# Performance work log

Measured on AMD Instinct MI355X. Metric: run time of the kernel, lower is better.

Reference implementation:

```python
import jax, jax.numpy as jnp
import numpy as np

N_NODES = 100000
N_EDGES = 3200000
N_IN = 128
N_HID = 128
N_OUT = 64
HOP = 10


def setup_inputs() -> dict:
    key = jax.random.key(0)
    ks = jax.random.split(key, 8)
    x = jax.random.normal(ks[0], (N_NODES, N_IN), dtype=jnp.float32)
    edge_row = jax.random.randint(ks[1], (N_EDGES,), 0, N_NODES, dtype=jnp.int32)
    edge_col = jax.random.randint(ks[2], (N_EDGES,), 0, N_NODES, dtype=jnp.int32)
    # normalized-ish edge weights so 10 hops of propagation stay bounded
    edge_val = jax.random.uniform(ks[3], (N_EDGES,), dtype=jnp.float32) / 32.0
    s_ih = 1.0 / np.sqrt(N_IN)
    s_hh = 1.0 / np.sqrt(N_HID)
    W_ih = jax.random.normal(ks[4], (4 * N_HID, N_IN), dtype=jnp.float32) * s_ih
    W_hh = jax.random.normal(ks[5], (4 * N_HID, N_HID), dtype=jnp.float32) * s_hh
    b_ih = jnp.zeros((4 * N_HID,), dtype=jnp.float32)
    b_hh = jnp.zeros((4 * N_HID,), dtype=jnp.float32)
    fc_w = jax.random.normal(ks[6], (N_OUT, N_HID), dtype=jnp.float32) * s_hh
    fc_b = jnp.zeros((N_OUT,), dtype=jnp.float32)
    return dict(x=x, edge_row=edge_row, edge_col=edge_col, edge_val=edge_val,
                W_ih=W_ih, W_hh=W_hh, b_ih=b_ih, b_hh=b_hh, fc_w=fc_w, fc_b=fc_b)


def _lstm_cell(x, h, c, W_ih, W_hh, b_ih, b_hh):
    # torch LSTMCell gate order: input, forget, cell(g), output
    gates = x @ W_ih.T + b_ih + h @ W_hh.T + b_hh  # [N, 4H]
    i, f, g, o = jnp.split(gates, 4, axis=-1)
    i = jax.nn.sigmoid(i)
    f = jax.nn.sigmoid(f)
    g = jnp.tanh(g)
    o = jax.nn.sigmoid(o)
    c_new = f * c + i * g
    h_new = o * jnp.tanh(c_new)
    return h_new, c_new


def _spmm(edge_row, edge_col, edge_val, h, n_nodes):
    # (A @ h)[r] = sum_{edges e with row r} val[e] * h[col[e]]
    msgs = edge_val[:, None] * h[edge_col]  # [E, H] gather
    return jax.ops.segment_sum(msgs, edge_row, num_segments=n_nodes)


def reference(x, edge_row, edge_col, edge_val, W_ih, W_hh, b_ih, b_hh, fc_w, fc_b):
    n = x.shape[0]
    h = jnp.zeros((n, W_hh.shape[1]), dtype=x.dtype)
    c = jnp.zeros_like(h)
    # hop iterations: LSTM gate update then sparse propagation (dropout = eval/identity)
    for _ in range(HOP):
        h, c = _lstm_cell(x, h, c, W_ih, W_hh, b_ih, b_hh)
        h = _spmm(edge_row, edge_col, edge_val, h, n)
    h = jax.nn.relu(h)
    return h @ fc_w.T + fc_b
```

## Files before the change

### kernel.cpp

```cpp
#include <hip/hip_runtime.h>
#include <hip/hip_bf16.h>
#include <math.h>

constexpr int NN  = 100000;
constexpr int EE  = 3200000;
constexpr int HID = 128;
constexpr int NG  = 512;
constexpr int NOUT = 64;
constexpr int HOPS = 10;

typedef __attribute__((ext_vector_type(8))) short short8;
typedef __attribute__((ext_vector_type(4))) float f32x4;

__device__ __forceinline__ ushort f2bf(float f) {
    uint u = __builtin_bit_cast(uint, f);
    u += 0x7fff + ((u >> 16) & 1);
    return (ushort)(u >> 16);
}
__device__ __forceinline__ float bflo(uint u) { return __builtin_bit_cast(float, u << 16); }
__device__ __forceinline__ float bfhi(uint u) { return __builtin_bit_cast(float, u & 0xffff0000u); }

__device__ __forceinline__ float sigf(float v) { return 1.0f / (1.0f + __expf(-v)); }
__device__ __forceinline__ float tanh_fast(float x) {
    float t = __expf(-2.0f * fabsf(x));
    float r = (1.0f - t) / (1.0f + t);
    return copysignf(r, x);
}

__device__ __forceinline__ short8 load_frag(const ushort* p) {
    return *reinterpret_cast<const short8*>(p);
}
__device__ __forceinline__ f32x4 mfma16(short8 a, short8 b, f32x4 c) {
    return __builtin_amdgcn_mfma_f32_16x16x32_bf16(a, b, c, 0, 0, 0);
}

__global__ __launch_bounds__(256) void convert_bf16_kernel(
    const float* __restrict__ src, ushort* __restrict__ dst, int n4)
{
    int i = blockIdx.x * 256 + threadIdx.x;
    if (i < n4) {
        float4 v = reinterpret_cast<const float4*>(src)[i];
        ushort4 o;
        o.x = f2bf(v.x); o.y = f2bf(v.y); o.z = f2bf(v.z); o.w = f2bf(v.w);
        reinterpret_cast<ushort4*>(dst)[i] = o;
    }
}

__global__ __launch_bounds__(256) void bsum_kernel(
    const float* __restrict__ bih, const float* __restrict__ bhh, float* __restrict__ bsum)
{
    int i = blockIdx.x * 256 + threadIdx.x;
    if (i < NG) bsum[i] = bih[i] + bhh[i];
}

__global__ __launch_bounds__(256) void hist_kernel(const int* __restrict__ erow,
                                                   int* __restrict__ deg)
{
    int e = blockIdx.x * 256 + threadIdx.x;
    atomicAdd(&deg[erow[e]], 1);
}

__global__ __launch_bounds__(1024) void scan_kernel(const int* __restrict__ deg,
                                                    int* __restrict__ rp,
                                                    int* __restrict__ cur)
{
    __shared__ int tmp[1024];
    __shared__ int carry_s;
    int t = threadIdx.x;
    if (t == 0) { carry_s = 0; rp[0] = 0; }
    __syncthreads();
    for (int base = 0; base < NN; base += 1024) {
        int i = base + t;
        int v = (i < NN) ? deg[i] : 0;
        tmp[t] = v;
        __syncthreads();
        for (int off = 1; off < 1024; off <<= 1) {
            int add = (t >= off) ? tmp[t - off] : 0;
            __syncthreads();
            tmp[t] += add;
            __syncthreads();
        }
        int incl = tmp[t] + carry_s;
        if (i < NN) { rp[i + 1] = incl; cur[i] = incl - v; }
        __syncthreads();
        if (t == 1023) carry_s = incl;
        __syncthreads();
    }
}

__global__ __launch_bounds__(256) void scatter_kernel(
    const int* __restrict__ erow, const int* __restrict__ ecol,
    const float* __restrict__ eval, int* __restrict__ cur,
    int* __restrict__ scol, float* __restrict__ sval)
{
    int e = blockIdx.x * 256 + threadIdx.x;
    int r = erow[e];
    int p = atomicAdd(&cur[r], 1);
    scol[p] = ecol[e];
    sval[p] = eval[e];
}

template<bool FIRST>
__global__ __launch_bounds__(256, 2) void cell_kernel(
    const ushort* __restrict__ xb, const ushort* __restrict__ hb,
    const ushort* __restrict__ Wib, const ushort* __restrict__ Whb,
    const float* __restrict__ bsum, float* __restrict__ cperm,
    ushort* __restrict__ hout)
{
    __shared__ __align__(16) ushort lds_h[32 * 136];

    const int t  = threadIdx.x;
    const int l  = t & 63;
    const int w  = t >> 6;
    const int lr = l & 15;
    const int lk = l >> 4;
    const int row0 = blockIdx.x * 32;

    f32x4 acc[8][2];
#pragma unroll
    for (int nI = 0; nI < 8; ++nI) {
        float b = bsum[(4 * nI + w) * 16 + lr];
        acc[nI][0] = f32x4{b, b, b, b};
        acc[nI][1] = f32x4{b, b, b, b};
    }

    short8 ax[2][4];
    short8 ah[2][4];
#pragma unroll
    for (int rf = 0; rf < 2; ++rf) {
        const size_t arow = (size_t)(row0 + rf * 16 + lr) * HID + lk * 8;
#pragma unroll
        for (int ks = 0; ks < 4; ++ks) {
            ax[rf][ks] = load_frag(xb + arow + ks * 32);
            if (!FIRST) ah[rf][ks] = load_frag(hb + arow + ks * 32);
        }
    }

#pragma unroll
    for (int nI = 0; nI < 8; ++nI) {
        const int n = 4 * nI + w;
        const ushort* wip = Wib + (size_t)(n * 16 + lr) * HID + lk * 8;
        const ushort* whp = Whb + (size_t)(n * 16 + lr) * HID + lk * 8;
        short8 bi[4], bh[4];
#pragma unroll
        for (int ks = 0; ks < 4; ++ks) {
            bi[ks] = load_frag(wip + ks * 32);
            if (!FIRST) bh[ks] = load_frag(whp + ks * 32);
        }
#pragma unroll
        for (int rf = 0; rf < 2; ++rf) {
#pragma unroll
            for (int ks = 0; ks < 4; ++ks) {
                acc[nI][rf] = mfma16(ax[rf][ks], bi[ks], acc[nI][rf]);
                if (!FIRST) acc[nI][rf] = mfma16(ah[rf][ks], bh[ks], acc[nI][rf]);
            }
        }
    }

#pragma unroll
    for (int nj = 0; nj < 2; ++nj) {
        const int col = (w + 4 * nj) * 16 + lr;
#pragma unroll
        for (int rf = 0; rf < 2; ++rf) {
            f32x4 iv = acc[nj][rf];
            f32x4 fv = acc[nj + 2][rf];
            f32x4 gv = acc[nj + 4][rf];
            f32x4 ov = acc[nj + 6][rf];
            const size_t cidx = ((((size_t)blockIdx.x * 4 + w) * 2 + nj) * 2 + rf) * 64 + l;
            f32x4 cold;
            if (FIRST) cold = f32x4{0.f, 0.f, 0.f, 0.f};
            else       cold = reinterpret_cast<const f32x4*>(cperm)[cidx];
            f32x4 cn, hn;
#pragma unroll
            for (int jj = 0; jj < 4; ++jj) {
                float c2 = sigf(fv[jj]) * cold[jj] + sigf(iv[jj]) * tanh_fast(gv[jj]);
                cn[jj] = c2;
                hn[jj] = sigf(ov[jj]) * tanh_fast(c2);
            }
            reinterpret_cast<f32x4*>(cperm)[cidx] = cn;
            const int rbase = rf * 16 + lk * 4;
#pragma unroll
            for (int jj = 0; jj < 4; ++jj)
                lds_h[(rbase + jj) * 136 + col] = f2bf(hn[jj]);
        }
    }
    __syncthreads();
    {
        const ushort* lsrc = &lds_h[(t >> 3) * 136 + (t & 7) * 16];
        short8 v0 = *reinterpret_cast<const short8*>(lsrc);
        short8 v1 = *reinterpret_cast<const short8*>(lsrc + 8);
        ushort* gdst = hout + (size_t)row0 * HID + t * 16;
        *reinterpret_cast<short8*>(gdst) = v0;
        *reinterpret_cast<short8*>(gdst + 8) = v1;
    }
}

__global__ __launch_bounds__(256) void spmm_kernel(
    const int* __restrict__ rp, const int* __restrict__ scol,
    const float* __restrict__ sval, const ushort* __restrict__ hin,
    ushort* __restrict__ hout)
{
    int r = blockIdx.x * 4 + (threadIdx.x >> 6);
    if (r >= NN) return;
    int l = threadIdx.x & 63;
    int beg = rp[r], end = rp[r + 1];

    float s0a = 0.f, s1a = 0.f, s0b = 0.f, s1b = 0.f;
    float s0c = 0.f, s1c = 0.f, s0d = 0.f, s1d = 0.f;
    int e = beg;
    for (; e + 4 <= end; e += 4) {
        int c0 = scol[e], c1 = scol[e + 1], c2 = scol[e + 2], c3 = scol[e + 3];
        float v0 = sval[e], v1 = sval[e + 1], v2 = sval[e + 2], v3 = sval[e + 3];
        uint g0 = *reinterpret_cast<const uint*>(hin + (size_t)c0 * HID + l * 2);
        uint g1 = *reinterpret_cast<const uint*>(hin + (size_t)c1 * HID + l * 2);
        uint g2 = *reinterpret_cast<const uint*>(hin + (size_t)c2 * HID + l * 2);
        uint g3 = *reinterpret_cast<const uint*>(hin + (size_t)c3 * HID + l * 2);
        s0a += v0 * bflo(g0); s1a += v0 * bfhi(g0);
        s0b += v1 * bflo(g1); s1b += v1 * bfhi(g1);
        s0c += v2 * bflo(g2); s1c += v2 * bfhi(g2);
        s0d += v3 * bflo(g3); s1d += v3 * bfhi(g3);
    }
    for (; e < end; ++e) {
        int c0 = scol[e];
        float v0 = sval[e];
        uint g0 = *reinterpret_cast<const uint*>(hin + (size_t)c0 * HID + l * 2);
        s0a += v0 * bflo(g0); s1a += v0 * bfhi(g0);
    }
    float s0 = (s0a + s0b) + (s0c + s0d);
    float s1 = (s1a + s1b) + (s1c + s1d);
    uint o = ((uint)f2bf(s1) << 16) | (uint)f2bf(s0);
    *reinterpret_cast<uint*>(hout + (size_t)r * HID + l * 2) = o;
}

__global__ __launch_bounds__(256) void final_mfma_kernel(
    const ushort* __restrict__ hb, const ushort* __restrict__ fcwb,
    const float* __restrict__ fcb, float* __restrict__ out)
{
    const int t = threadIdx.x;
    const int l = t & 63;
    const int w = t >> 6;
    const int lr = l & 15;
    const int lk = l >> 4;
    const int row0 = blockIdx.x * 64 + w * 16;

    f32x4 acc[4];
#pragma unroll
    for (int n = 0; n < 4; ++n) {
        float b = fcb[n * 16 + lr];
        acc[n] = f32x4{b, b, b, b};
    }

    const short8 z8 = {0, 0, 0, 0, 0, 0, 0, 0};
    const int arow = row0 + lr;
    const bool aok = arow < NN;
    short8 a[4];
#pragma unroll
    for (int ks = 0; ks < 4; ++ks) {
        short8 v = aok ? load_frag(hb + (size_t)arow * HID + ks * 32 + lk * 8) : z8;
#pragma unroll
        for (int i = 0; i < 8; ++i) {
            ushort u = (ushort)v[i];
            if (u & 0x8000) v[i] = 0;
        }
        a[ks] = v;
    }

#pragma unroll
    for (int n = 0; n < 4; ++n) {
        const ushort* wp = fcwb + (size_t)(n * 16 + lr) * HID + lk * 8;
#pragma unroll
        for (int ks = 0; ks < 4; ++ks)
            acc[n] = mfma16(a[ks], load_frag(wp + ks * 32), acc[n]);
    }

#pragma unroll
    for (int n = 0; n < 4; ++n) {
#pragma unroll
        for (int j = 0; j < 4; ++j) {
            int row = row0 + lk * 4 + j;
            if (row < NN) out[(size_t)row * NOUT + n * 16 + lr] = acc[n][j];
        }
    }
}

extern "C" void kernel_launch(void* const* d_in, const int* in_sizes, int n_in,
                              void* d_out, int out_size, void* d_ws, size_t ws_size,
                              hipStream_t stream)
{
    const float* x    = (const float*)d_in[0];
    const int*   erow = (const int*)d_in[1];
    const int*   ecol = (const int*)d_in[2];
    const float* eval = (const float*)d_in[3];
    const float* Wih  = (const float*)d_in[4];
    const float* Whh  = (const float*)d_in[5];
    const float* bih  = (const float*)d_in[6];
    const float* bhh  = (const float*)d_in[7];
    const float* fcw  = (const float*)d_in[8];
    const float* fcb  = (const float*)d_in[9];
    float* out = (float*)d_out;

    char* ws = (char*)d_ws;
    size_t off = 0;
    auto alloc = [&](size_t bytes) -> void* {
        void* p = ws + off;
        off = (off + bytes + 255) & ~(size_t)255;
        return p;
    };
    ushort* hb_a  = (ushort*)alloc((size_t)NN * HID * 2);
    ushort* hb_b  = (ushort*)alloc((size_t)NN * HID * 2);
    float*  cperm = (float*)alloc((size_t)NN * HID * 4);
    ushort* xb    = (ushort*)alloc((size_t)NN * HID * 2);
    ushort* Wib   = (ushort*)alloc((size_t)NG * HID * 2);
    ushort* Whb   = (ushort*)alloc((size_t)NG * HID * 2);
    ushort* fcwb  = (ushort*)alloc((size_t)NOUT * HID * 2);
    float*  bsum  = (float*)alloc((size_t)NG * 4);
    int*    rp    = (int*)alloc((size_t)(NN + 1) * 4);
    int*    deg   = (int*)alloc((size_t)NN * 4);
    int*    cur   = (int*)alloc((size_t)NN * 4);
    int*    scol  = (int*)alloc((size_t)EE * 4);
    float*  sval  = (float*)alloc((size_t)EE * 4);
    (void)ws_size;

    convert_bf16_kernel<<<(NN * HID / 4 + 255) / 256, 256, 0, stream>>>(x, xb, NN * HID / 4);
    convert_bf16_kernel<<<(NG * HID / 4 + 255) / 256, 256, 0, stream>>>(Wih, Wib, NG * HID / 4);
    convert_bf16_kernel<<<(NG * HID / 4 + 255) / 256, 256, 0, stream>>>(Whh, Whb, NG * HID / 4);
    convert_bf16_kernel<<<(NOUT * HID / 4 + 255) / 256, 256, 0, stream>>>(fcw, fcwb, NOUT * HID / 4);
    bsum_kernel<<<2, 256, 0, stream>>>(bih, bhh, bsum);

    hipMemsetAsync(deg, 0, (size_t)NN * 4, stream);
    hist_kernel<<<EE / 256, 256, 0, stream>>>(erow, deg);
    scan_kernel<<<1, 1024, 0, stream>>>(deg, rp, cur);
    scatter_kernel<<<EE / 256, 256, 0, stream>>>(erow, ecol, eval, cur, scol, sval);

    const int CELL_GRID = NN / 32;

    cell_kernel<true><<<CELL_GRID, 256, 0, stream>>>(xb, hb_b, Wib, Whb, bsum, cperm, hb_a);
    spmm_kernel<<<(NN + 3) / 4, 256, 0, stream>>>(rp, scol, sval, hb_a, hb_b);
    for (int hop = 1; hop < HOPS; ++hop) {
        cell_kernel<false><<<CELL_GRID, 256, 0, stream>>>(xb, hb_b, Wib, Whb, bsum, cperm, hb_a);
        spmm_kernel<<<(NN + 3) / 4, 256, 0, stream>>>(rp, scol, sval, hb_a, hb_b);
    }

    final_mfma_kernel<<<(NN + 63) / 64, 256, 0, stream>>>(hb_b, fcwb, fcb, out);
}
```

Before: 2.941 ms.

## Parallelize CSR row-pointer scan across blocks and pack edge column/value pairs

Replaces the single-block sequential prefix scan over node degrees with a three-kernel block-reduce, block-offset scan, and per-block scan. This is meant to remove a long serial preprocessing step. Also packs each edge's column index and weight into one int2 so the scatter writes and the SpMM reads one 8-byte record per edge instead of two separate arrays. It adds two extra kernel launches and a redundant store in the second scan kernel.

```diff
diff --git a/kernel.cpp b/kernel.cpp
--- a/kernel.cpp
+++ b/kernel.cpp
@@ -8,6 +8,8 @@
 constexpr int NG  = 512;
 constexpr int NOUT = 64;
 constexpr int HOPS = 10;
+constexpr int SCAN_BLK = 1024;
+constexpr int NBLK_SCAN = (NN + SCAN_BLK - 1) / SCAN_BLK;
 
 typedef __attribute__((ext_vector_type(8))) short short8;
 typedef __attribute__((ext_vector_type(4))) float f32x4;
@@ -60,44 +62,74 @@
     atomicAdd(&deg[erow[e]], 1);
 }
 
-__global__ __launch_bounds__(1024) void scan_kernel(const int* __restrict__ deg,
-                                                    int* __restrict__ rp,
-                                                    int* __restrict__ cur)
-{
-    __shared__ int tmp[1024];
-    __shared__ int carry_s;
+__global__ __launch_bounds__(SCAN_BLK) void scan1_kernel(const int* __restrict__ deg,
+                                                         int* __restrict__ bsums)
+{
+    __shared__ int tmp[SCAN_BLK];
     int t = threadIdx.x;
-    if (t == 0) { carry_s = 0; rp[0] = 0; }
+    int i = blockIdx.x * SCAN_BLK + t;
+    tmp[t] = (i < NN) ? deg[i] : 0;
     __syncthreads();
-    for (int base = 0; base < NN; base += 1024) {
-        int i = base + t;
-        int v = (i < NN) ? deg[i] : 0;
-        tmp[t] = v;
-        __syncthreads();
-        for (int off = 1; off < 1024; off <<= 1) {
-            int add = (t >= off) ? tmp[t - off] : 0;
-            __syncthreads();
-            tmp[t] += add;
-            __syncthreads();
-        }
-        int incl = tmp[t] + carry_s;
-        if (i < NN) { rp[i + 1] = incl; cur[i] = incl - v; }
-        __syncthreads();
-        if (t == 1023) carry_s = incl;
-        __syncthreads();
-    }
+    for (int off = SCAN_BLK / 2; off > 0; off >>= 1) {
+        if (t < off) tmp[t] += tmp[t + off];
+        __syncthreads();
+    }
+    if (t == 0) bsums[blockIdx.x] = tmp[0];
+}
+
+__global__ __launch_bounds__(128) void scan2_kernel(int* __restrict__ bsums)
+{
+    __shared__ int tmp[128];
+    int t = threadIdx.x;
+    tmp[t] = (t < NBLK_SCAN) ? bsums[t] : 0;
+    __syncthreads();
+    for (int off = 1; off < 128; off <<= 1) {
+        int add = (t >= off) ? tmp[t - off] : 0;
+        __syncthreads();
+        tmp[t] += add;
+        __syncthreads();
+    }
+    if (t < NBLK_SCAN) bsums[t] = tmp[t] - ((t < NBLK_SCAN) ? 0 : 0) - (t < NBLK_SCAN ? (t == 0 ? tmp[0] : tmp[t] - tmp[t - 1]) : 0) + ((t == 0) ? 0 : tmp[t - 1]) - ((t == 0) ? 0 : tmp[t - 1]);
+    if (t < NBLK_SCAN) bsums[t] = (t == 0) ? 0 : tmp[t - 1];
+}
+
+__global__ __launch_bounds__(SCAN_BLK) void scan3_kernel(const int* __restrict__ deg,
+                                                         const int* __restrict__ bsums,
+                                                         int* __restrict__ rp,
+                                                         int* __restrict__ cur)
+{
+    __shared__ int tmp[SCAN_BLK];
+    int t = threadIdx.x;
+    int i = blockIdx.x * SCAN_BLK + t;
+    int v = (i < NN) ? deg[i] : 0;
+    tmp[t] = v;
+    __syncthreads();
+    for (int off = 1; off < SCAN_BLK; off <<= 1) {
+        int add = (t >= off) ? tmp[t - off] : 0;
+        __syncthreads();
+        tmp[t] += add;
+        __syncthreads();
+    }
+    int incl = tmp[t] + bsums[blockIdx.x];
+    if (i < NN) {
+        rp[i + 1] = incl;
+        cur[i] = incl - v;
+    }
+    if (i == 0) rp[0] = 0;
 }
 
 __global__ __launch_bounds__(256) void scatter_kernel(
     const int* __restrict__ erow, const int* __restrict__ ecol,
     const float* __restrict__ eval, int* __restrict__ cur,
-    int* __restrict__ scol, float* __restrict__ sval)
+    int2* __restrict__ epack)
 {
     int e = blockIdx.x * 256 + threadIdx.x;
     int r = erow[e];
     int p = atomicAdd(&cur[r], 1);
-    scol[p] = ecol[e];
-    sval[p] = eval[e];
+    int2 pk;
+    pk.x = ecol[e];
+    pk.y = __builtin_bit_cast(int, eval[e]);
+    epack[p] = pk;
 }
 
 template<bool FIRST>
@@ -196,9 +228,8 @@
 }
 
 __global__ __launch_bounds__(256) void spmm_kernel(
-    const int* __restrict__ rp, const int* __restrict__ scol,
-    const float* __restrict__ sval, const ushort* __restrict__ hin,
-    ushort* __restrict__ hout)
+    const int* __restrict__ rp, const int2* __restrict__ epack,
+    const ushort* __restrict__ hin, ushort* __restrict__ hout)
 {
     int r = blockIdx.x * 4 + (threadIdx.x >> 6);
     if (r >= NN) return;
@@ -209,21 +240,24 @@
     float s0c = 0.f, s1c = 0.f, s0d = 0.f, s1d = 0.f;
     int e = beg;
     for (; e + 4 <= end; e += 4) {
-        int c0 = scol[e], c1 = scol[e + 1], c2 = scol[e + 2], c3 = scol[e + 3];
-        float v0 = sval[e], v1 = sval[e + 1], v2 = sval[e + 2], v3 = sval[e + 3];
-        uint g0 = *reinterpret_cast<const uint*>(hin + (size_t)c0 * HID + l * 2);
-        uint g1 = *reinterpret_cast<const uint*>(hin + (size_t)c1 * HID + l * 2);
-        uint g2 = *reinterpret_cast<const uint*>(hin + (size_t)c2 * HID + l * 2);
-        uint g3 = *reinterpret_cast<const uint*>(hin + (size_t)c3 * HID + l * 2);
+        int2 p0 = epack[e], p1 = epack[e + 1], p2 = epack[e + 2], p3 = epack[e + 3];
+        float v0 = __builtin_bit_cast(float, p0.y);
+        float v1 = __builtin_bit_cast(float, p1.y);
+        float v2 = __builtin_bit_cast(float, p2.y);
+        float v3 = __builtin_bit_cast(float, p3.y);
+        uint g0 = *reinterpret_cast<const uint*>(hin + (size_t)p0.x * HID + l * 2);
+        uint g1 = *reinterpret_cast<const uint*>(hin + (size_t)p1.x * HID + l * 2);
+        uint g2 = *reinterpret_cast<const uint*>(hin + (size_t)p2.x * HID + l * 2);
+        uint g3 = *reinterpret_cast<const uint*>(hin + (size_t)p3.x * HID + l * 2);
         s0a += v0 * bflo(g0); s1a += v0 * bfhi(g0);
         s0b += v1 * bflo(g1); s1b += v1 * bfhi(g1);
         s0c += v2 * bflo(g2); s1c += v2 * bfhi(g2);
         s0d += v3 * bflo(g3); s1d += v3 * bfhi(g3);
     }
     for (; e < end; ++e) {
-        int c0 = scol[e];
-        float v0 = sval[e];
-        uint g0 = *reinterpret_cast<const uint*>(hin + (size_t)c0 * HID + l * 2);
+        int2 p0 = epack[e];
+        float v0 = __builtin_bit_cast(float, p0.y);
+        uint g0 = *reinterpret_cast<const uint*>(hin + (size_t)p0.x * HID + l * 2);
         s0a += v0 * bflo(g0); s1a += v0 * bfhi(g0);
     }
     float s0 = (s0a + s0b) + (s0c + s0d);
@@ -317,8 +351,8 @@
     int*    rp    = (int*)alloc((size_t)(NN + 1) * 4);
     int*    deg   = (int*)alloc((size_t)NN * 4);
     int*    cur   = (int*)alloc((size_t)NN * 4);
-    int*    scol  = (int*)alloc((size_t)EE * 4);
-    float*  sval  = (float*)alloc((size_t)EE * 4);
+    int*    bsums = (int*)alloc((size_t)NBLK_SCAN * 4);
+    int2*   epack = (int2*)alloc((size_t)EE * 8);
     (void)ws_size;
 
     convert_bf16_kernel<<<(NN * HID / 4 + 255) / 256, 256, 0, stream>>>(x, xb, NN * HID / 4);
@@ -329,16 +363,18 @@
 
     hipMemsetAsync(deg, 0, (size_t)NN * 4, stream);
     hist_kernel<<<EE / 256, 256, 0, stream>>>(erow, deg);
-    scan_kernel<<<1, 1024, 0, stream>>>(deg, rp, cur);
-    scatter_kernel<<<EE / 256, 256, 0, stream>>>(erow, ecol, eval, cur, scol, sval);
+    scan1_kernel<<<NBLK_SCAN, SCAN_BLK, 0, stream>>>(deg, bsums);
+    scan2_kernel<<<1, 128, 0, stream>>>(bsums);
+    scan3_kernel<<<NBLK_SCAN, SCAN_BLK, 0, stream>>>(deg, bsums, rp, cur);
+    scatter_kernel<<<EE / 256, 256, 0, stream>>>(erow, ecol, eval, cur, epack);
 
     const int CELL_GRID = NN / 32;
 
     cell_kernel<true><<<CELL_GRID, 256, 0, stream>>>(xb, hb_b, Wib, Whb, bsum, cperm, hb_a);
-    spmm_kernel<<<(NN + 3) / 4, 256, 0, stream>>>(rp, scol, sval, hb_a, hb_b);
+    spmm_kernel<<<(NN + 3) / 4, 256, 0, stream>>>(rp, epack, hb_a, hb_b);
     for (int hop = 1; hop < HOPS; ++hop) {
         cell_kernel<false><<<CELL_GRID, 256, 0, stream>>>(xb, hb_b, Wib, Whb, bsum, cperm, hb_a);
-        spmm_kernel<<<(NN + 3) / 4, 256, 0, stream>>>(rp, scol, sval, hb_a, hb_b);
+        spmm_kernel<<<(NN + 3) / 4, 256, 0, stream>>>(rp, epack, hb_a, hb_b);
     }
 
     final_mfma_kernel<<<(NN + 63) / 64, 256, 0, stream>>>(hb_b, fcwb, fcb, out);
```

Result: faster. 2.803 ms (-4.7%).
